# Kernel optimization log

Hardware: AMD Instinct MI355X
Metric: run time of the kernel (lower is better)

Reference implementation:

```python
import jax, jax.numpy as jnp
import numpy as np

N_NODES = 100000
N_EDGES = 1000000
HIDDEN = 64
IN_DIM = 4


def setup_inputs() -> dict:
    key = jax.random.key(0)
    ks = jax.random.split(key, 7)
    x = jax.random.normal(ks[0], (N_NODES, IN_DIM), dtype=jnp.float32)
    edges = jax.random.randint(ks[1], (N_EDGES, 2), 0, N_NODES, dtype=jnp.int32)
    W1 = jax.random.normal(ks[2], (IN_DIM, HIDDEN), dtype=jnp.float32) * 0.5
    b1 = jax.random.normal(ks[3], (HIDDEN,), dtype=jnp.float32) * 0.1
    phases = jax.random.normal(ks[4], (N_EDGES,), dtype=jnp.float32) * 0.1
    Wout = jax.random.normal(ks[5], (HIDDEN, 1), dtype=jnp.float32) * 0.1
    bout = jax.random.normal(ks[6], (1,), dtype=jnp.float32) * 0.1
    return {"x": x, "edges": edges, "W1": W1, "b1": b1,
            "phases": phases, "Wout": Wout, "bout": bout}


def reference(x, edges, W1, b1, phases, Wout, bout):
    # h = lin(x): [N, D]
    h = x @ W1 + b1
    u = edges[:, 0]  # [E]
    v = edges[:, 1]  # [E]
    c = jnp.cos(phases)  # [E]
    s = jnp.sin(phases)  # [E]
    hu = h[u]  # [E, D] gather
    hv = h[v]  # [E, D] gather
    # rot only mixes the first two channels; the rest pass through (eye).
    # msg to v: rot @ h[u] -> [c*h0 - s*h1, s*h0 + c*h1, h2, ...]
    msg_v = jnp.concatenate([
        (c * hu[:, 0] - s * hu[:, 1])[:, None],
        (s * hu[:, 0] + c * hu[:, 1])[:, None],
        hu[:, 2:],
    ], axis=1)
    # msg to u: rot.T @ h[v] -> [c*h0 + s*h1, -s*h0 + c*h1, h2, ...]
    msg_u = jnp.concatenate([
        (c * hv[:, 0] + s * hv[:, 1])[:, None],
        (-s * hv[:, 0] + c * hv[:, 1])[:, None],
        hv[:, 2:],
    ], axis=1)
    diffused = jnp.zeros_like(h).at[v].add(msg_v).at[u].add(msg_u)  # scatter-add
    return (h + diffused) @ Wout + bout  # [N, 1]
```

## Files before the change

### kernel.cpp

```cpp
#include <hip/hip_runtime.h>

#define N_NODES 100000
#define N_EDGES 1000000
#define HIDDEN 64

#define N_RANGES 8
#define C_RANGE 13312
#define N_SLICES 64
#define ES (N_EDGES / N_SLICES)
#define CH 2048
#define NC ((ES + CH - 1) / CH)
#define QCAP 704
#define A_THREADS 512

__device__ __forceinline__ void compute_consts(
    const float* __restrict__ W1, const float* __restrict__ b1,
    const float* __restrict__ Wout, const float* __restrict__ bout,
    float* kc, int tid) {
    if (tid < 64) {
        float wj = Wout[tid];
        float p0 = W1[0 * HIDDEN + tid] * wj;
        float p1 = W1[1 * HIDDEN + tid] * wj;
        float p2 = W1[2 * HIDDEN + tid] * wj;
        float p3 = W1[3 * HIDDEN + tid] * wj;
        float pb = b1[tid] * wj;
        #pragma unroll
        for (int off = 32; off > 0; off >>= 1) {
            p0 += __shfl_down(p0, off);
            p1 += __shfl_down(p1, off);
            p2 += __shfl_down(p2, off);
            p3 += __shfl_down(p3, off);
            pb += __shfl_down(pb, off);
        }
        if (tid < 4) {
            kc[5 + tid] = W1[tid * HIDDEN + 0];
            kc[9 + tid] = W1[tid * HIDDEN + 1];
        }
        if (tid == 0) {
            kc[0] = p0; kc[1] = p1; kc[2] = p2; kc[3] = p3; kc[4] = pb;
            kc[13] = b1[0]; kc[14] = b1[1];
            kc[15] = Wout[0]; kc[16] = Wout[1];
            kc[17] = bout[0];
        }
    }
}

__device__ __forceinline__ float contrib(
    float4 xe, float cs, float sn_signed,
    float c0, float c1, float c2, float c3, float cb,
    float a0, float a1, float a2, float a3,
    float g0, float g1, float g2, float g3,
    float b10, float b11, float w0, float w1) {
    float h0 = xe.x * a0 + xe.y * a1 + xe.z * a2 + xe.w * a3 + b10;
    float h1 = xe.x * g0 + xe.y * g1 + xe.z * g2 + xe.w * g3 + b11;
    float d  = xe.x * c0 + xe.y * c1 + xe.z * c2 + xe.w * c3 + cb;
    float a  = h0 * w0 + h1 * w1;
    float b  = h0 * w1 - h1 * w0;
    return cs * a + sn_signed * b + (d - a);
}

__global__ __launch_bounds__(A_THREADS) void range_kernel(
    const int2* __restrict__ edges, const float* __restrict__ phases,
    const float4* __restrict__ x4,
    const float* __restrict__ W1, const float* __restrict__ b1,
    const float* __restrict__ Wout, const float* __restrict__ bout,
    float* __restrict__ part) {
    __shared__ float bins[C_RANGE];
    __shared__ uint2 qbuf[2][QCAP];
    __shared__ int   qcnt[2];
    __shared__ int   qn_sh[2];
    __shared__ float kc[18];
    const int tid = threadIdx.x;
    const int r = blockIdx.x >> 6;
    const int s = blockIdx.x & 63;

    compute_consts(W1, b1, Wout, bout, kc, tid);
    for (int j = tid; j < C_RANGE; j += A_THREADS) bins[j] = 0.0f;
    if (tid < 2) { qcnt[tid] = 0; qn_sh[tid] = 0; }
    __syncthreads();

    const float c0 = kc[0], c1 = kc[1], c2 = kc[2], c3 = kc[3], cb = kc[4];
    const float a0 = kc[5], a1 = kc[6], a2 = kc[7], a3 = kc[8];
    const float g0 = kc[9], g1 = kc[10], g2 = kc[11], g3 = kc[12];
    const float b10 = kc[13], b11 = kc[14], w0 = kc[15], w1 = kc[16];

    const int nlo = r * C_RANGE;
    const int e0 = s * ES;

    auto scan_push = [&](int cc, int dstb) {
        const int ebase = e0 + cc * CH;
        const int eend  = min(ebase + CH, e0 + ES);
        for (int e = ebase + tid; e < eend; e += A_THREADS) {
            int2 ed = edges[e];
            float ph = phases[e];
            unsigned jv = (unsigned)(ed.y - nlo);
            unsigned ju = (unsigned)(ed.x - nlo);
            if (jv < C_RANGE) {
                int pos = atomicAdd(&qcnt[dstb], 1);
                if (pos < QCAP)
                    qbuf[dstb][pos] = make_uint2(jv | ((unsigned)ed.x << 15),
                                                 __float_as_uint(ph));
            }
            if (ju < C_RANGE) {
                int pos = atomicAdd(&qcnt[dstb], 1);
                if (pos < QCAP)
                    qbuf[dstb][pos] = make_uint2(ju | 0x4000u | ((unsigned)ed.y << 15),
                                                 __float_as_uint(ph));
            }
        }
    };

    scan_push(0, 0);
    __syncthreads();
    if (tid == 0) { qn_sh[0] = min(qcnt[0], QCAP); qcnt[0] = 0; }
    __syncthreads();

    for (int c = 0; c < NC; c++) {
        const int curb = c & 1, pb = curb ^ 1;
        if (c + 1 < NC) scan_push(c + 1, pb);
        const int qn = qn_sh[curb];
        for (int q = tid; q < qn; q += A_THREADS) {
            uint2 it = qbuf[curb][q];
            unsigned pk = it.x;
            int dest = pk & 0x3FFFu;
            float sg = (pk & 0x4000u) ? -1.0f : 1.0f;
            int src = pk >> 15;
            float ph = __uint_as_float(it.y);
            float sn, cs;
            __sincosf(ph, &sn, &cs);
            float4 xs = x4[src];
            float val = contrib(xs, cs, sg * sn, c0, c1, c2, c3, cb,
                                a0, a1, a2, a3, g0, g1, g2, g3, b10, b11, w0, w1);
            atomicAdd(&bins[dest], val);
        }
        __syncthreads();
        if (tid == 0) { qn_sh[pb] = min(qcnt[pb], QCAP); qcnt[pb] = 0; }
        __syncthreads();
    }

    float* __restrict__ dst = part + (size_t)blockIdx.x * C_RANGE;
    for (int j = tid; j < C_RANGE; j += A_THREADS) dst[j] = bins[j];
}

__global__ __launch_bounds__(A_THREADS) void reduce_kernel(
    const float4* __restrict__ x4,
    const float* __restrict__ W1, const float* __restrict__ b1,
    const float* __restrict__ Wout, const float* __restrict__ bout,
    const float* __restrict__ part, float* __restrict__ out) {
    __shared__ float kc[18];
    compute_consts(W1, b1, Wout, bout, kc, threadIdx.x);
    __syncthreads();
    int i = blockIdx.x * A_THREADS + threadIdx.x;
    if (i >= N_NODES) return;
    int r = i / C_RANGE;
    int j = i - r * C_RANGE;
    const float* __restrict__ p = part + ((size_t)r * N_SLICES) * C_RANGE + j;
    float sum = 0.0f;
    #pragma unroll 16
    for (int s = 0; s < N_SLICES; s++) sum += p[(size_t)s * C_RANGE];
    float4 xi = x4[i];
    out[i] = sum + xi.x * kc[0] + xi.y * kc[1] + xi.z * kc[2] + xi.w * kc[3]
           + kc[4] + kc[17];
}

__global__ void precompute_kernel(const float* __restrict__ W1,
                                  const float* __restrict__ b1,
                                  const float* __restrict__ Wout,
                                  const float* __restrict__ bout,
                                  float* __restrict__ consts) {
    __shared__ float kc[18];
    compute_consts(W1, b1, Wout, bout, kc, threadIdx.x);
    __syncthreads();
    if (threadIdx.x < 18) consts[threadIdx.x] = kc[threadIdx.x];
}

__global__ void edge_atomic_kernel(const int2* __restrict__ edges,
                                   const float* __restrict__ phases,
                                   const float4* __restrict__ x4,
                                   const float* __restrict__ consts,
                                   float* __restrict__ rep) {
    int e = blockIdx.x * blockDim.x + threadIdx.x;
    if (e >= N_EDGES) return;
    float c0 = consts[0], c1 = consts[1], c2 = consts[2], c3 = consts[3];
    float cb = consts[4];
    float a0 = consts[5], a1 = consts[6], a2 = consts[7], a3 = consts[8];
    float g0 = consts[9], g1 = consts[10], g2 = consts[11], g3 = consts[12];
    float b10 = consts[13], b11 = consts[14], w0 = consts[15], w1 = consts[16];
    int2 ed = edges[e];
    float ph = phases[e];
    float sn, cs;
    __sincosf(ph, &sn, &cs);
    float4 xu = x4[ed.x];
    float4 xv = x4[ed.y];
    atomicAdd(rep + ed.y, contrib(xu, cs,  sn, c0,c1,c2,c3,cb, a0,a1,a2,a3, g0,g1,g2,g3, b10,b11,w0,w1));
    atomicAdd(rep + ed.x, contrib(xv, cs, -sn, c0,c1,c2,c3,cb, a0,a1,a2,a3, g0,g1,g2,g3, b10,b11,w0,w1));
}

__global__ void final_kernel(const float4* __restrict__ x4,
                             const float* __restrict__ consts,
                             const float* __restrict__ rep,
                             float* __restrict__ out) {
    int i = blockIdx.x * blockDim.x + threadIdx.x;
    if (i >= N_NODES) return;
    float4 xi = x4[i];
    out[i] = rep[i] + xi.x * consts[0] + xi.y * consts[1] + xi.z * consts[2]
           + xi.w * consts[3] + consts[4] + consts[17];
}

extern "C" void kernel_launch(void* const* d_in, const int* in_sizes, int n_in,
                              void* d_out, int out_size, void* d_ws, size_t ws_size,
                              hipStream_t stream) {
    const float* x      = (const float*)d_in[0];
    const int*   edges  = (const int*)d_in[1];
    const float* W1     = (const float*)d_in[2];
    const float* b1     = (const float*)d_in[3];
    const float* phases = (const float*)d_in[4];
    const float* Wout   = (const float*)d_in[5];
    const float* bout   = (const float*)d_in[6];
    float* out = (float*)d_out;

    const size_t part_bytes =
        (size_t)N_RANGES * N_SLICES * C_RANGE * sizeof(float);

    if (ws_size >= part_bytes) {
        float* part = (float*)d_ws;
        range_kernel<<<N_RANGES * N_SLICES, A_THREADS, 0, stream>>>(
            (const int2*)edges, phases, (const float4*)x,
            W1, b1, Wout, bout, part);
        reduce_kernel<<<(N_NODES + A_THREADS - 1) / A_THREADS, A_THREADS, 0, stream>>>(
            (const float4*)x, W1, b1, Wout, bout, part, out);
    } else {
        float* consts = (float*)d_ws;
        float* rep    = (float*)((char*)d_ws + 256);
        hipMemsetAsync(rep, 0, N_NODES * sizeof(float), stream);
        precompute_kernel<<<1, 64, 0, stream>>>(W1, b1, Wout, bout, consts);
        edge_atomic_kernel<<<(N_EDGES + 255) / 256, 256, 0, stream>>>(
            (const int2*)edges, phases, (const float4*)x, consts, rep);
        final_kernel<<<(N_NODES + 255) / 256, 256, 0, stream>>>(
            (const float4*)x, consts, rep, out);
    }
}
```

Before: 111.7 us.

## Replace block-wide double-buffered edge queue with per-wave ballot compaction buffers

Each wave now filters its edges into a private shared-memory buffer. It uses ballot and popcount prefix offsets instead of block-wide atomic counters, and processes 64 queued items whenever the buffer fills. This removes the per-chunk __syncthreads barriers and LDS atomic contention on the queue counter, and it drops the QCAP overflow cap that could lose edges. The node range per block shrinks so 8 ranges just cover all nodes, which cuts partial-buffer writes and LDS use. Bin zeroing and copy-out now use float4. Per-wave processing in 64-item batches can leave lanes unbalanced at the tail, and it relies on explicit lgkmcnt waits for intra-wave LDS visibility.

```diff
diff --git a/kernel.cpp b/kernel.cpp
--- a/kernel.cpp
+++ b/kernel.cpp
@@ -5,13 +5,13 @@
 #define HIDDEN 64
 
 #define N_RANGES 8
-#define C_RANGE 13312
+#define C_RANGE 12544
 #define N_SLICES 64
 #define ES (N_EDGES / N_SLICES)
-#define CH 2048
-#define NC ((ES + CH - 1) / CH)
-#define QCAP 704
 #define A_THREADS 512
+#define WAVES (A_THREADS / 64)
+#define BUFCAP 128
+#define A_GRID (N_RANGES * N_SLICES)
 
 __device__ __forceinline__ void compute_consts(
     const float* __restrict__ W1, const float* __restrict__ b1,
@@ -66,17 +66,20 @@
     const float* __restrict__ Wout, const float* __restrict__ bout,
     float* __restrict__ part) {
     __shared__ float bins[C_RANGE];
-    __shared__ uint2 qbuf[2][QCAP];
-    __shared__ int   qcnt[2];
-    __shared__ int   qn_sh[2];
+    __shared__ uint2 wbuf[WAVES][BUFCAP];
     __shared__ float kc[18];
-    const int tid = threadIdx.x;
-    const int r = blockIdx.x >> 6;
-    const int s = blockIdx.x & 63;
+    const int tid  = threadIdx.x;
+    const int lane = tid & 63;
+    const int w    = tid >> 6;
+    const int r    = blockIdx.x >> 6;
+    const int s    = blockIdx.x & 63;
 
     compute_consts(W1, b1, Wout, bout, kc, tid);
-    for (int j = tid; j < C_RANGE; j += A_THREADS) bins[j] = 0.0f;
-    if (tid < 2) { qcnt[tid] = 0; qn_sh[tid] = 0; }
+    {
+        float4 z = make_float4(0.f, 0.f, 0.f, 0.f);
+        float4* b4 = (float4*)bins;
+        for (int j = tid; j < C_RANGE / 4; j += A_THREADS) b4[j] = z;
+    }
     __syncthreads();
 
     const float c0 = kc[0], c1 = kc[1], c2 = kc[2], c3 = kc[3], cb = kc[4];
@@ -85,61 +88,62 @@
     const float b10 = kc[13], b11 = kc[14], w0 = kc[15], w1 = kc[16];
 
     const int nlo = r * C_RANGE;
-    const int e0 = s * ES;
-
-    auto scan_push = [&](int cc, int dstb) {
-        const int ebase = e0 + cc * CH;
-        const int eend  = min(ebase + CH, e0 + ES);
-        for (int e = ebase + tid; e < eend; e += A_THREADS) {
-            int2 ed = edges[e];
-            float ph = phases[e];
-            unsigned jv = (unsigned)(ed.y - nlo);
-            unsigned ju = (unsigned)(ed.x - nlo);
-            if (jv < C_RANGE) {
-                int pos = atomicAdd(&qcnt[dstb], 1);
-                if (pos < QCAP)
-                    qbuf[dstb][pos] = make_uint2(jv | ((unsigned)ed.x << 15),
-                                                 __float_as_uint(ph));
-            }
-            if (ju < C_RANGE) {
-                int pos = atomicAdd(&qcnt[dstb], 1);
-                if (pos < QCAP)
-                    qbuf[dstb][pos] = make_uint2(ju | 0x4000u | ((unsigned)ed.y << 15),
-                                                 __float_as_uint(ph));
-            }
-        }
+    const int e0 = s * ES, e1 = e0 + ES;
+    uint2* __restrict__ buf = wbuf[w];
+    int cnt = 0;
+    const unsigned long long lml = (1ull << lane) - 1ull;
+
+    auto process = [&](uint2 it) {
+        unsigned pk = it.x;
+        int dest = pk & 0x3FFFu;
+        float sg = (pk & 0x4000u) ? -1.0f : 1.0f;
+        int src = pk >> 15;
+        float sn, cs;
+        __sincosf(__uint_as_float(it.y), &sn, &cs);
+        float4 xs = x4[src];
+        float val = contrib(xs, cs, sg * sn, c0, c1, c2, c3, cb,
+                            a0, a1, a2, a3, g0, g1, g2, g3, b10, b11, w0, w1);
+        atomicAdd(&bins[dest], val);
     };
 
-    scan_push(0, 0);
-    __syncthreads();
-    if (tid == 0) { qn_sh[0] = min(qcnt[0], QCAP); qcnt[0] = 0; }
-    __syncthreads();
-
-    for (int c = 0; c < NC; c++) {
-        const int curb = c & 1, pb = curb ^ 1;
-        if (c + 1 < NC) scan_push(c + 1, pb);
-        const int qn = qn_sh[curb];
-        for (int q = tid; q < qn; q += A_THREADS) {
-            uint2 it = qbuf[curb][q];
-            unsigned pk = it.x;
-            int dest = pk & 0x3FFFu;
-            float sg = (pk & 0x4000u) ? -1.0f : 1.0f;
-            int src = pk >> 15;
-            float ph = __uint_as_float(it.y);
-            float sn, cs;
-            __sincosf(ph, &sn, &cs);
-            float4 xs = x4[src];
-            float val = contrib(xs, cs, sg * sn, c0, c1, c2, c3, cb,
-                                a0, a1, a2, a3, g0, g1, g2, g3, b10, b11, w0, w1);
-            atomicAdd(&bins[dest], val);
-        }
-        __syncthreads();
-        if (tid == 0) { qn_sh[pb] = min(qcnt[pb], QCAP); qcnt[pb] = 0; }
-        __syncthreads();
-    }
-
-    float* __restrict__ dst = part + (size_t)blockIdx.x * C_RANGE;
-    for (int j = tid; j < C_RANGE; j += A_THREADS) dst[j] = bins[j];
+    for (int base = e0 + w * 64; base < e1; base += A_THREADS) {
+        int e = base + lane;
+        bool inb = e < e1;
+        int eload = inb ? e : (N_EDGES - 1);
+        int2 ed = edges[eload];
+        float ph = phases[eload];
+        unsigned jv = (unsigned)(ed.y - nlo);
+        unsigned ju = (unsigned)(ed.x - nlo);
+        bool pv = inb && (jv < C_RANGE);
+        bool pu = inb && (ju < C_RANGE);
+
+        unsigned long long mv = __ballot(pv);
+        if (pv) buf[cnt + __popcll(mv & lml)] =
+            make_uint2(jv | ((unsigned)ed.x << 15), __float_as_uint(ph));
+        cnt += __popcll(mv);
+        if (cnt >= 64) {
+            cnt -= 64;
+            asm volatile("s_waitcnt lgkmcnt(0)" ::: "memory");
+            process(buf[cnt + lane]);
+        }
+
+        unsigned long long mu = __ballot(pu);
+        if (pu) buf[cnt + __popcll(mu & lml)] =
+            make_uint2(ju | 0x4000u | ((unsigned)ed.y << 15), __float_as_uint(ph));
+        cnt += __popcll(mu);
+        if (cnt >= 64) {
+            cnt -= 64;
+            asm volatile("s_waitcnt lgkmcnt(0)" ::: "memory");
+            process(buf[cnt + lane]);
+        }
+    }
+    asm volatile("s_waitcnt lgkmcnt(0)" ::: "memory");
+    if (lane < cnt) process(buf[lane]);
+
+    __syncthreads();
+    float4* __restrict__ d4 = (float4*)(part + (size_t)blockIdx.x * C_RANGE);
+    const float4* b4 = (const float4*)bins;
+    for (int j = tid; j < C_RANGE / 4; j += A_THREADS) d4[j] = b4[j];
 }
 
 __global__ __launch_bounds__(A_THREADS) void reduce_kernel(
@@ -220,11 +224,11 @@
     float* out = (float*)d_out;
 
     const size_t part_bytes =
-        (size_t)N_RANGES * N_SLICES * C_RANGE * sizeof(float);
+        (size_t)A_GRID * C_RANGE * sizeof(float);
 
     if (ws_size >= part_bytes) {
         float* part = (float*)d_ws;
-        range_kernel<<<N_RANGES * N_SLICES, A_THREADS, 0, stream>>>(
+        range_kernel<<<A_GRID, A_THREADS, 0, stream>>>(
             (const int2*)edges, phases, (const float4*)x,
             W1, b1, Wout, bout, part);
         reduce_kernel<<<(N_NODES + A_THREADS - 1) / A_THREADS, A_THREADS, 0, stream>>>(
```

New measurement: 105.2 us. -5.8%, faster.
